# Kernel tuning notes

Measured on AMD Instinct MI355X. Metric: run time of the kernel, lower is better.

Reference implementation:

```python
import jax, jax.numpy as jnp
import numpy as np

DEPTH = 4
DIM = 1024
HEADS = 16
DIM_HEAD = 64
BLOCK = 128
FF_HID = 2730  # int(1024 * 4.0 * 2 / 3)
EPS = 1.1920929e-07  # torch float32 finfo eps (nn.RMSNorm default)
SCALE = DIM_HEAD ** -0.5


def rmsnorm(x, w):
    return x * jax.lax.rsqrt(jnp.mean(x * x, axis=-1, keepdims=True) + EPS) * w


def rope(x):
    # interleaved rotary embedding (rotary-embedding-torch convention)
    n, d = x.shape[-2], x.shape[-1]
    freqs = 1.0 / (10000.0 ** (jnp.arange(0, d, 2, dtype=jnp.float32) / d))  # [d/2]
    ang = jnp.arange(n, dtype=jnp.float32)[:, None] * freqs                  # [n, d/2]
    cos = jnp.repeat(jnp.cos(ang), 2, axis=-1)  # [n, d], interleaved
    sin = jnp.repeat(jnp.sin(ang), 2, axis=-1)
    xp = x.reshape(x.shape[:-1] + (d // 2, 2))
    xr = jnp.stack((-xp[..., 1], xp[..., 0]), axis=-1).reshape(x.shape)
    return x * cos + xr * sin


def setup_inputs() -> dict:
    key = jax.random.key(0)
    ks = jax.random.split(key, 8)
    g = lambda k, shape: jax.random.normal(k, shape, jnp.float32) * 0.02
    return dict(
        tokens=jax.random.normal(ks[0], (1, 2048, DIM), jnp.float32),
        attn_norm_w=jnp.ones((DEPTH, DIM), jnp.float32),
        w_qkv=g(ks[1], (DEPTH, DIM, 3 * HEADS * DIM_HEAD)),
        w_attn_out=g(ks[2], (DEPTH, HEADS * DIM_HEAD, DIM)),
        w_mix=g(ks[3], (DEPTH, DIM, HEADS)),
        b_mix=jnp.zeros((DEPTH, HEADS), jnp.float32),
        ff_norm_w=jnp.ones((DEPTH, DIM), jnp.float32),
        w_ff_in=g(ks[4], (DEPTH, DIM, 2 * FF_HID)),
        b_ff_in=jnp.zeros((DEPTH, 2 * FF_HID), jnp.float32),
        w_ff_out=g(ks[5], (DEPTH, FF_HID, DIM)),
        b_ff_out=jnp.zeros((DEPTH, DIM), jnp.float32),
        final_norm_w=jnp.ones((DIM,), jnp.float32),
    )


def reference(tokens, attn_norm_w, w_qkv, w_attn_out, w_mix, b_mix,
              ff_norm_w, w_ff_in, b_ff_in, w_ff_out, b_ff_out, final_norm_w):
    b, n, _ = tokens.shape
    qi = jnp.arange(n) // BLOCK
    mask = qi[:, None] >= qi[None, :]  # block-causal [n, n]
    neg = -jnp.finfo(jnp.float32).max

    def split_heads(t):
        return t.reshape(b, n, HEADS, DIM_HEAD).transpose(0, 2, 1, 3)  # b h n d

    x = tokens
    first_v = None
    for i in range(DEPTH):
        # --- block-causal attention ---
        h = rmsnorm(x, attn_norm_w[i])
        q, k, v = jnp.split(h @ w_qkv[i], 3, axis=-1)
        q, k, v = split_heads(q), split_heads(k), split_heads(v)
        orig_v = v
        q, k = rope(q), rope(k)
        if first_v is not None:
            mix = jax.nn.sigmoid(h @ w_mix[i] + b_mix[i])      # b n h
            mix = mix.transpose(0, 2, 1)[..., None]            # b h n 1
            v = v + mix * (first_v - v)                        # lerp
        sim = jnp.einsum('bhid,bhjd->bhij', q * SCALE, k)
        sim = jnp.where(mask, sim, neg)
        attn = jax.nn.softmax(sim, axis=-1)
        o = jnp.einsum('bhij,bhjd->bhid', attn, v)
        o = o.transpose(0, 2, 1, 3).reshape(b, n, HEADS * DIM_HEAD)
        x = x + o @ w_attn_out[i]
        if first_v is None:
            first_v = orig_v
        # --- SwiGLU feedforward ---
        hf = rmsnorm(x, ff_norm_w[i])
        a, g_ = jnp.split(hf @ w_ff_in[i] + b_ff_in[i], 2, axis=-1)
        x = x + (a * jax.nn.gelu(g_, approximate=False)) @ w_ff_out[i] + b_ff_out[i]

    return rmsnorm(x, final_norm_w)
```

## Files before the change

kernel.cpp:

```cpp
#include <hip/hip_runtime.h>
#include <hip/hip_bf16.h>

#define DIM   1024
#define NTOK  2048
#define HEADS 16
#define FFH   2730
#define FF2   5460
#define FFHP  2752
#define FFNP  2816
#define DEPTH 4
#define EPS_RMS 1.1920929e-07f
#define QK_SCALE 0.125f

typedef __attribute__((ext_vector_type(8))) short bf16x8;
typedef __attribute__((ext_vector_type(4))) float f32x4;

__device__ __forceinline__ unsigned short f2bf(float x) {
    unsigned u = __float_as_uint(x);
    u += 0x7fffu + ((u >> 16) & 1);
    return (unsigned short)(u >> 16);
}
__device__ __forceinline__ float bf2f(unsigned short u) {
    return __uint_as_float((unsigned)u << 16);
}
__device__ __forceinline__ unsigned pk2(float a, float b) {
    unsigned ua = __float_as_uint(a); ua += 0x7fffu + ((ua >> 16) & 1);
    unsigned ub = __float_as_uint(b); ub += 0x7fffu + ((ub >> 16) & 1);
    return (ua >> 16) | (ub & 0xffff0000u);
}
__device__ __forceinline__ void gll16(const void* g, void* l) {
    __builtin_amdgcn_global_load_lds(
        (const __attribute__((address_space(1))) void*)g,
        (__attribute__((address_space(3))) void*)l, 16, 0, 0);
}

__global__ void rmsnorm_k(const float* __restrict__ in, const float* __restrict__ w,
                          unsigned short* __restrict__ outbf) {
    int row = blockIdx.x;
    int tid = threadIdx.x;
    const float4* in4 = (const float4*)(in + (size_t)row * DIM);
    float4 v = in4[tid];
    float ss = v.x * v.x + v.y * v.y + v.z * v.z + v.w * v.w;
    #pragma unroll
    for (int off = 32; off > 0; off >>= 1) ss += __shfl_down(ss, off);
    __shared__ float lds[4];
    __shared__ float stot;
    int wid = tid >> 6, lane = tid & 63;
    if (lane == 0) lds[wid] = ss;
    __syncthreads();
    if (tid == 0) stot = lds[0] + lds[1] + lds[2] + lds[3];
    __syncthreads();
    float inv = 1.0f / sqrtf(stot * (1.0f / DIM) + EPS_RMS);
    const float4* w4 = (const float4*)w;
    float4 wv = w4[tid];
    float4 o;
    o.x = v.x * inv * wv.x; o.y = v.y * inv * wv.y;
    o.z = v.z * inv * wv.z; o.w = v.w * inv * wv.w;
    unsigned long long p = (unsigned long long)pk2(o.x, o.y)
                         | ((unsigned long long)pk2(o.z, o.w) << 32);
    ((unsigned long long*)(outbf + (size_t)row * DIM))[tid] = p;
}

template<int S, int DOMIX>
__global__ void rmsnorm_red_k(const float* __restrict__ X,
                              const unsigned short* __restrict__ P,
                              const float* __restrict__ bias, const float* __restrict__ w,
                              float* __restrict__ Xout, float* __restrict__ Hf,
                              unsigned short* __restrict__ Hbf,
                              const float* __restrict__ wm, const float* __restrict__ bm,
                              float* __restrict__ mix) {
    int row = blockIdx.x;
    int tid = threadIdx.x;
    float4 x = ((const float4*)(X + (size_t)row * DIM))[tid];
    #pragma unroll
    for (int s = 0; s < S; s++) {
        ushort4 p = ((const ushort4*)(P + (size_t)s * NTOK * DIM + (size_t)row * DIM))[tid];
        x.x += bf2f(p.x); x.y += bf2f(p.y); x.z += bf2f(p.z); x.w += bf2f(p.w);
    }
    if (bias) {
        float4 b = ((const float4*)bias)[tid];
        x.x += b.x; x.y += b.y; x.z += b.z; x.w += b.w;
    }
    float ss = x.x * x.x + x.y * x.y + x.z * x.z + x.w * x.w;
    #pragma unroll
    for (int off = 32; off > 0; off >>= 1) ss += __shfl_down(ss, off);
    __shared__ float lds[4];
    __shared__ float stot;
    int wid = tid >> 6, lane = tid & 63;
    if (lane == 0) lds[wid] = ss;
    __syncthreads();
    if (tid == 0) stot = lds[0] + lds[1] + lds[2] + lds[3];
    __syncthreads();
    float inv = 1.0f / sqrtf(stot * (1.0f / DIM) + EPS_RMS);
    if (Xout) ((float4*)(Xout + (size_t)row * DIM))[tid] = x;
    float4 wv = ((const float4*)w)[tid];
    float4 o;
    o.x = x.x * inv * wv.x; o.y = x.y * inv * wv.y;
    o.z = x.z * inv * wv.z; o.w = x.w * inv * wv.w;
    if (Hf) ((float4*)(Hf + (size_t)row * DIM))[tid] = o;
    if (Hbf) {
        unsigned long long p = (unsigned long long)pk2(o.x, o.y)
                             | ((unsigned long long)pk2(o.z, o.w) << 32);
        ((unsigned long long*)(Hbf + (size_t)row * DIM))[tid] = p;
    }
    if (DOMIX) {
        __shared__ float olds[1024];
        __shared__ float red[256];
        ((float4*)olds)[tid] = o;
        __syncthreads();
        int hh = tid & 15, kl = tid >> 4;
        float pm = 0.f;
        #pragma unroll
        for (int j = 0; j < 64; j++) {
            int k = kl + 16 * j;
            pm += olds[k] * wm[k * 16 + hh];
        }
        red[tid] = pm;
        __syncthreads();
        if (tid < 16) {
            float s = 0.f;
            #pragma unroll
            for (int k2 = 0; k2 < 16; k2++) s += red[k2 * 16 + tid];
            s += bm[tid];
            mix[row * HEADS + tid] = 1.0f / (1.0f + expf(-s));
        }
    }
}

__global__ __launch_bounds__(256) void wconv_k(
        const float* __restrict__ W0, short* __restrict__ out0,
        int Ksrc, int Nsrc, int colOfs, int rowStride, int Kp, int Np,
        size_t wStride, size_t oStride) {
    const float* W = W0 + (size_t)blockIdx.z * wStride;
    short* out = out0 + (size_t)blockIdx.z * oStride;
    __shared__ float tile[64][65];
    int k0 = blockIdx.y * 64, n0 = blockIdx.x * 64;
    int tid = threadIdx.x;
    int c = tid & 63;
    #pragma unroll
    for (int kk4 = 0; kk4 < 16; kk4++) {
        int kk = kk4 * 4 + (tid >> 6);
        int gk = k0 + kk, gn = n0 + c;
        float v = 0.f;
        if (gk < Ksrc && gn < Nsrc) v = W[(size_t)gk * rowStride + colOfs + gn];
        tile[kk][c] = v;
    }
    __syncthreads();
    #pragma unroll
    for (int it = 0; it < 4; it++) {
        int flat = tid + 256 * it;
        int nn = flat >> 4, kg = (flat & 15) * 4;
        int gn = n0 + nn, gk = k0 + kg;
        if (gn < Np && gk < Kp) {
            short4 s;
            s.x = (short)f2bf(tile[kg + 0][nn]);
            s.y = (short)f2bf(tile[kg + 1][nn]);
            s.z = (short)f2bf(tile[kg + 2][nn]);
            s.w = (short)f2bf(tile[kg + 3][nn]);
            *(short4*)(out + (size_t)gn * Kp + gk) = s;
        }
    }
}

template<int SPLITK, int OUT16>
__global__ __launch_bounds__(256, 2) void gemm_splitk_k(
        const short* __restrict__ A, const short* __restrict__ Bt,
        void* __restrict__ Cpart, int N, int Kp) {
    __shared__ __align__(16) short As[128 * 64];
    __shared__ __align__(16) short Bs[128 * 64];
    int tid = threadIdx.x;
    int wv = tid >> 6, ln = tid & 63, g = ln >> 4, t = ln & 15;
    int wr = wv >> 1, wc = wv & 1;
    int rowBase = blockIdx.y * 128, colBase = blockIdx.x * 128;
    f32x4 acc[4][4] = {};
    int KT = Kp >> 6;
    int kt0 = (KT * blockIdx.z) / SPLITK, kt1 = (KT * (blockIdx.z + 1)) / SPLITK;
    for (int kt = kt0; kt < kt1; kt++) {
        int k0 = kt * 64;
        #pragma unroll
        for (int i = 0; i < 4; i++) {
            int idx = tid + 256 * i;
            int r = idx >> 3, c8 = idx & 7;
            int cs = (c8 ^ (r & 7)) * 8;
            gll16(A + (size_t)(rowBase + r) * Kp + k0 + cs, (char*)As + idx * 16);
            gll16(Bt + (size_t)(colBase + r) * Kp + k0 + cs, (char*)Bs + idx * 16);
        }
        __syncthreads();
        #pragma unroll
        for (int ks = 0; ks < 2; ks++) {
            bf16x8 af[4], bf[4];
            #pragma unroll
            for (int mi = 0; mi < 4; mi++) {
                int row = wr * 64 + mi * 16 + t;
                int kb = (ks * 64 + g * 16) ^ ((row & 7) << 4);
                af[mi] = *(const bf16x8*)((const char*)As + row * 128 + kb);
            }
            #pragma unroll
            for (int ni = 0; ni < 4; ni++) {
                int row = wc * 64 + ni * 16 + t;
                int kb = (ks * 64 + g * 16) ^ ((row & 7) << 4);
                bf[ni] = *(const bf16x8*)((const char*)Bs + row * 128 + kb);
            }
            #pragma unroll
            for (int mi = 0; mi < 4; mi++)
                #pragma unroll
                for (int ni = 0; ni < 4; ni++)
                    acc[mi][ni] = __builtin_amdgcn_mfma_f32_16x16x32_bf16(
                        af[mi], bf[ni], acc[mi][ni], 0, 0, 0);
        }
        __syncthreads();
    }
    #pragma unroll
    for (int mi = 0; mi < 4; mi++)
        #pragma unroll
        for (int ni = 0; ni < 4; ni++) {
            int col = colBase + wc * 64 + ni * 16 + t;
            #pragma unroll
            for (int r = 0; r < 4; r++) {
                int row = rowBase + wr * 64 + mi * 16 + g * 4 + r;
                if (OUT16) {
                    unsigned short* Cz = (unsigned short*)Cpart
                                       + (size_t)blockIdx.z * NTOK * N;
                    Cz[(size_t)row * N + col] = f2bf(acc[mi][ni][r]);
                } else {
                    float* Cz = (float*)Cpart + (size_t)blockIdx.z * NTOK * N;
                    Cz[(size_t)row * N + col] = acc[mi][ni][r];
                }
            }
        }
}

__global__ __launch_bounds__(256, 2) void gemm_swiglu_k(
        const short* __restrict__ A, const short* __restrict__ Ba,
        const short* __restrict__ Bg, const float* __restrict__ biasIn,
        unsigned short* __restrict__ actbf) {
    __shared__ __align__(16) short As[128 * 64];
    __shared__ __align__(16) short B1[128 * 64];
    __shared__ __align__(16) short B2[128 * 64];
    int tid = threadIdx.x;
    int wv = tid >> 6, ln = tid & 63, g = ln >> 4, t = ln & 15;
    int wr = wv >> 1, wc = wv & 1;
    int rowBase = blockIdx.y * 128, colBase = blockIdx.x * 128;
    f32x4 acca[4][4] = {};
    f32x4 accg[4][4] = {};
    for (int kt = 0; kt < 16; kt++) {
        int k0 = kt * 64;
        #pragma unroll
        for (int i = 0; i < 4; i++) {
            int idx = tid + 256 * i;
            int r = idx >> 3, c8 = idx & 7;
            int cs = (c8 ^ (r & 7)) * 8;
            gll16(A + (size_t)(rowBase + r) * 1024 + k0 + cs, (char*)As + idx * 16);
            gll16(Ba + (size_t)(colBase + r) * 1024 + k0 + cs, (char*)B1 + idx * 16);
            gll16(Bg + (size_t)(colBase + r) * 1024 + k0 + cs, (char*)B2 + idx * 16);
        }
        __syncthreads();
        #pragma unroll
        for (int ks = 0; ks < 2; ks++) {
            bf16x8 af[4], b1f[4], b2f[4];
            #pragma unroll
            for (int mi = 0; mi < 4; mi++) {
                int row = wr * 64 + mi * 16 + t;
                int kb = (ks * 64 + g * 16) ^ ((row & 7) << 4);
                af[mi] = *(const bf16x8*)((const char*)As + row * 128 + kb);
            }
            #pragma unroll
            for (int ni = 0; ni < 4; ni++) {
                int row = wc * 64 + ni * 16 + t;
                int kb = (ks * 64 + g * 16) ^ ((row & 7) << 4);
                b1f[ni] = *(const bf16x8*)((const char*)B1 + row * 128 + kb);
                b2f[ni] = *(const bf16x8*)((const char*)B2 + row * 128 + kb);
            }
            #pragma unroll
            for (int mi = 0; mi < 4; mi++)
                #pragma unroll
                for (int ni = 0; ni < 4; ni++) {
                    acca[mi][ni] = __builtin_amdgcn_mfma_f32_16x16x32_bf16(
                        af[mi], b1f[ni], acca[mi][ni], 0, 0, 0);
                    accg[mi][ni] = __builtin_amdgcn_mfma_f32_16x16x32_bf16(
                        af[mi], b2f[ni], accg[mi][ni], 0, 0, 0);
                }
        }
        __syncthreads();
    }
    const float rs2 = 0.70710678118654752f;
    #pragma unroll
    for (int mi = 0; mi < 4; mi++)
        #pragma unroll
        for (int ni = 0; ni < 4; ni++) {
            int col = colBase + wc * 64 + ni * 16 + t;
            if (col < FFHP) {
                float ba = (col < FFH) ? biasIn[col] : 0.f;
                float bg = (col < FFH) ? biasIn[FFH + col] : 0.f;
                #pragma unroll
                for (int r = 0; r < 4; r++) {
                    int row = rowBase + wr * 64 + mi * 16 + g * 4 + r;
                    unsigned short outv = 0;
                    if (col < FFH) {
                        float a_ = acca[mi][ni][r] + ba;
                        float g_ = accg[mi][ni][r] + bg;
                        float gel = 0.5f * g_ * (1.0f + erff(g_ * rs2));
                        outv = f2bf(a_ * gel);
                    }
                    actbf[(size_t)row * FFHP + col] = outv;
                }
            }
        }
}

__global__ void rope_lerp_k(const float* __restrict__ qkv,
                            unsigned short* __restrict__ qbf,
                            unsigned short* __restrict__ kbf) {
    int row = blockIdx.x;
    int tid = threadIdx.x;
    const float* qr = qkv + (size_t)row * 3072;
    #pragma unroll
    for (int it = 0; it < 2; it++) {
        int p = tid + 256 * it;
        int hh = p >> 5, pr = p & 31;
        float freq = expf(-(float)pr * (1.0f / 32.0f) * 9.2103403719762f);
        float ang = (float)row * freq;
        float s, c;
        sincosf(ang, &s, &c);
        int base = hh * 64 + pr * 2;
        float q0 = qr[base], q1 = qr[base + 1];
        float qa = q0 * c - q1 * s, qb = q1 * c + q0 * s;
        *(unsigned*)(qbf + (size_t)row * DIM + base) = pk2(qa * QK_SCALE, qb * QK_SCALE);
        float k0 = qr[1024 + base], k1 = qr[1024 + base + 1];
        *(unsigned*)(kbf + (size_t)row * DIM + base) = pk2(k0 * c - k1 * s, k1 * c + k0 * s);
    }
}

__global__ __launch_bounds__(256) void vtrans_k(
        const float* __restrict__ qkv, float* __restrict__ fv,
        const float* __restrict__ mix, unsigned short* __restrict__ vtg, int layer) {
    __shared__ __align__(16) short T[64 * 64];
    int h = blockIdx.x, n0 = blockIdx.y * 64;
    int tid = threadIdx.x;
    #pragma unroll
    for (int it = 0; it < 2; it++) {
        int flat = tid + 256 * it;
        int n = flat >> 3, d0 = (flat & 7) * 8;
        int row = n0 + n;
        const float* src = qkv + (size_t)row * 3072 + 2048 + h * 64 + d0;
        float4 u0 = *(const float4*)src;
        float4 u1 = *(const float4*)(src + 4);
        float vals[8] = {u0.x, u0.y, u0.z, u0.w, u1.x, u1.y, u1.z, u1.w};
        float* fvp = fv + (size_t)row * DIM + h * 64 + d0;
        if (layer == 0) {
            *(float4*)fvp = u0;
            *(float4*)(fvp + 4) = u1;
        } else {
            float m = mix[row * HEADS + h];
            float4 f0 = *(const float4*)fvp;
            float4 f1 = *(const float4*)(fvp + 4);
            float fvv[8] = {f0.x, f0.y, f0.z, f0.w, f1.x, f1.y, f1.z, f1.w};
            #pragma unroll
            for (int e = 0; e < 8; e++) vals[e] += m * (fvv[e] - vals[e]);
        }
        #pragma unroll
        for (int e = 0; e < 8; e++) {
            int d = d0 + e;
            *(short*)((char*)T + d * 128 + ((2 * n) ^ ((d & 7) << 4))) = (short)f2bf(vals[e]);
        }
    }
    __syncthreads();
    #pragma unroll
    for (int it = 0; it < 2; it++) {
        int flat = tid + 256 * it;
        int d = flat >> 3, nn0 = (flat & 7) * 8;
        uint4 v = *(const uint4*)((const char*)T + d * 128 + ((2 * nn0) ^ ((d & 7) << 4)));
        *(uint4*)(vtg + (size_t)(h * 64 + d) * NTOK + n0 + nn0) = v;
    }
}

__global__ __launch_bounds__(256, 2) void attn_mfma_k(
        const unsigned short* __restrict__ Qbf, const unsigned short* __restrict__ Kbf,
        const unsigned short* __restrict__ Vtg, unsigned short* __restrict__ obf) {
    const int h = blockIdx.x;
    const int j = 31 - (int)blockIdx.y;
    const int tid = threadIdx.x;
    const int wv = tid >> 6, ln = tid & 63, g = ln >> 4, t = ln & 15;
    __shared__ __align__(16) short KsB[2][64 * 64];
    __shared__ __align__(16) short VtB[2][64 * 64];
    __shared__ __align__(16) short Plds[4 * 16 * 64];
    char* pw = (char*)(Plds + wv * 1024);

    const int sr = ln >> 3;
    const int scol = (ln & 7) ^ sr;
    const int sbyte0 = (wv * 16 + sr) * 128 + (ln & 7) * 16;
    const int sbyte1 = sbyte0 + 8 * 128;
    const unsigned short* kgl0 = Kbf + (size_t)(wv * 16 + sr) * DIM + h * 64 + scol * 8;
    const unsigned short* kgl1 = kgl0 + 8 * DIM;
    const unsigned short* vgl0 = Vtg + (size_t)(h * 64 + wv * 16 + sr) * NTOK + scol * 8;
    const unsigned short* vgl1 = vgl0 + 8 * NTOK;

    const int nch = ((j >> 1) + 1) * 2;
    const int qbase = j * 64;
    const unsigned short* qrow = Qbf + (size_t)(qbase + wv * 16 + t) * DIM + h * 64;
    bf16x8 qf0 = *(const bf16x8*)(qrow + 8 * g);
    bf16x8 qf1 = *(const bf16x8*)(qrow + 32 + 8 * g);
    f32x4 acc_o[4] = {};
    float mrun = -3.0e38f, lrun = 0.f;
    uint4 rk0 = *(const uint4*)kgl0;
    uint4 rk1 = *(const uint4*)kgl1;
    uint4 rv0 = *(const uint4*)vgl0;
    uint4 rv1 = *(const uint4*)vgl1;
    for (int kc = 0; kc < nch; kc++) {
        const int cur = kc & 1;
        *(uint4*)((char*)KsB[cur] + sbyte0) = rk0;
        *(uint4*)((char*)KsB[cur] + sbyte1) = rk1;
        *(uint4*)((char*)VtB[cur] + sbyte0) = rv0;
        *(uint4*)((char*)VtB[cur] + sbyte1) = rv1;
        if (kc + 1 < nch) {
            rk0 = *(const uint4*)(kgl0 + (size_t)(kc + 1) * 64 * DIM);
            rk1 = *(const uint4*)(kgl1 + (size_t)(kc + 1) * 64 * DIM);
            rv0 = *(const uint4*)(vgl0 + (kc + 1) * 64);
            rv1 = *(const uint4*)(vgl1 + (kc + 1) * 64);
        }
        __syncthreads();
        const char* Kc = (const char*)KsB[cur];
        const char* Vc = (const char*)VtB[cur];
        f32x4 accs[4] = {};
        #pragma unroll
        for (int kf = 0; kf < 4; kf++) {
            int row = kf * 16 + t;
            int kb0 = (g * 16) ^ ((row & 7) << 4);
            int kb1 = (64 + g * 16) ^ ((row & 7) << 4);
            bf16x8 k0 = *(const bf16x8*)(Kc + row * 128 + kb0);
            bf16x8 k1 = *(const bf16x8*)(Kc + row * 128 + kb1);
            accs[kf] = __builtin_amdgcn_mfma_f32_16x16x32_bf16(k0, qf0, accs[kf], 0, 0, 0);
            accs[kf] = __builtin_amdgcn_mfma_f32_16x16x32_bf16(k1, qf1, accs[kf], 0, 0, 0);
        }
        float pm = -3.0e38f;
        #pragma unroll
        for (int kf = 0; kf < 4; kf++)
            #pragma unroll
            for (int r = 0; r < 4; r++) pm = fmaxf(pm, accs[kf][r]);
        pm = fmaxf(pm, __shfl_xor(pm, 16));
        pm = fmaxf(pm, __shfl_xor(pm, 32));
        float mnew = fmaxf(mrun, pm);
        float corr = __expf(mrun - mnew);
        mrun = mnew;
        float psum = 0.f;
        #pragma unroll
        for (int kf = 0; kf < 4; kf++)
            #pragma unroll
            for (int r = 0; r < 4; r++) {
                float pv = __expf(accs[kf][r] - mnew);
                accs[kf][r] = pv;
                psum += pv;
            }
        psum += __shfl_xor(psum, 16);
        psum += __shfl_xor(psum, 32);
        lrun = lrun * corr + psum;
        #pragma unroll
        for (int kf = 0; kf < 4; kf++)
            #pragma unroll
            for (int rp = 0; rp < 4; rp += 2) {
                unsigned pv = pk2(accs[kf][rp], accs[kf][rp + 1]);
                int boff = (t * 128 + (16 * kf + 4 * g + rp) * 2) ^ ((t & 7) << 4);
                *(unsigned*)(pw + boff) = pv;
            }
        float cr[4];
        #pragma unroll
        for (int r = 0; r < 4; r++) cr[r] = __shfl(corr, g * 4 + r);
        #pragma unroll
        for (int ni = 0; ni < 4; ni++)
            #pragma unroll
            for (int r = 0; r < 4; r++) acc_o[ni][r] *= cr[r];
        #pragma unroll
        for (int ks = 0; ks < 2; ks++) {
            bf16x8 pa = *(const bf16x8*)(pw + ((t * 128 + 64 * ks + 16 * g) ^ ((t & 7) << 4)));
            #pragma unroll
            for (int ni = 0; ni < 4; ni++) {
                int row = ni * 16 + t;
                int vb = (64 * ks + 16 * g) ^ ((row & 7) << 4);
                bf16x8 vbf = *(const bf16x8*)(Vc + row * 128 + vb);
                acc_o[ni] = __builtin_amdgcn_mfma_f32_16x16x32_bf16(pa, vbf, acc_o[ni], 0, 0, 0);
            }
        }
    }
    float inv = 1.0f / lrun;
    float ir[4];
    #pragma unroll
    for (int r = 0; r < 4; r++) ir[r] = __shfl(inv, g * 4 + r);
    #pragma unroll
    for (int ni = 0; ni < 4; ni++)
        #pragma unroll
        for (int r = 0; r < 4; r++) {
            int row = qbase + wv * 16 + g * 4 + r;
            int col = h * 64 + ni * 16 + t;
            obf[(size_t)row * DIM + col] = f2bf(acc_o[ni][r] * ir[r]);
        }
}

extern "C" void kernel_launch(void* const* d_in, const int* in_sizes, int n_in,
                              void* d_out, int out_size, void* d_ws, size_t ws_size,
                              hipStream_t stream) {
    const float* tokens       = (const float*)d_in[0];
    const float* attn_norm_w  = (const float*)d_in[1];
    const float* w_qkv        = (const float*)d_in[2];
    const float* w_attn_out   = (const float*)d_in[3];
    const float* w_mix        = (const float*)d_in[4];
    const float* b_mix        = (const float*)d_in[5];
    const float* ff_norm_w    = (const float*)d_in[6];
    const float* b_ff_in      = (const float*)d_in[8];
    const float* w_ff_in      = (const float*)d_in[7];
    const float* w_ff_out     = (const float*)d_in[9];
    const float* b_ff_out     = (const float*)d_in[10];
    const float* final_norm_w = (const float*)d_in[11];

    char* p = (char*)d_ws;
    auto alloc = [&](size_t bytes) {
        char* r = p;
        p += (bytes + 255) & ~(size_t)255;
        return r;
    };
    short* wq_t  = (short*)alloc(4ull * 3072 * 1024 * 2);
    short* wo_t  = (short*)alloc(4ull * 1024 * 1024 * 2);
    short* wfa_t = (short*)alloc(4ull * FFNP * 1024 * 2);
    short* wfg_t = (short*)alloc(4ull * FFNP * 1024 * 2);
    short* wfo_t = (short*)alloc(4ull * 1024 * FFHP * 2);
    float* PART  = (float*)alloc((size_t)NTOK * 3072 * 4);
    float* X     = (float*)alloc((size_t)NTOK * DIM * 4);
    float* FV    = (float*)alloc((size_t)NTOK * DIM * 4);
    float* MIX   = (float*)alloc((size_t)NTOK * HEADS * 4);
    short* Hbf   = (short*)alloc((size_t)NTOK * DIM * 2);
    short* Obf   = (short*)alloc((size_t)NTOK * DIM * 2);
    short* ACTbf = (short*)alloc((size_t)NTOK * FFHP * 2);
    unsigned short* Qbf = (unsigned short*)alloc((size_t)NTOK * DIM * 2);
    unsigned short* Kbf = (unsigned short*)alloc((size_t)NTOK * DIM * 2);
    unsigned short* Vtg = (unsigned short*)alloc((size_t)HEADS * 64 * NTOK * 2);
    float* QKVf = PART;
    unsigned short* PARTb = (unsigned short*)PART;

    wconv_k<<<dim3(48, 16, 4), 256, 0, stream>>>(
        w_qkv, wq_t, 1024, 3072, 0, 3072, 1024, 3072,
        (size_t)1024 * 3072, (size_t)3072 * 1024);
    wconv_k<<<dim3(16, 16, 4), 256, 0, stream>>>(
        w_attn_out, wo_t, 1024, 1024, 0, 1024, 1024, 1024,
        (size_t)1024 * 1024, (size_t)1024 * 1024);
    wconv_k<<<dim3(44, 16, 4), 256, 0, stream>>>(
        w_ff_in, wfa_t, 1024, FFH, 0, FF2, 1024, FFNP,
        (size_t)1024 * FF2, (size_t)FFNP * 1024);
    wconv_k<<<dim3(44, 16, 4), 256, 0, stream>>>(
        w_ff_in, wfg_t, 1024, FFH, FFH, FF2, 1024, FFNP,
        (size_t)1024 * FF2, (size_t)FFNP * 1024);
    wconv_k<<<dim3(16, 43, 4), 256, 0, stream>>>(
        w_ff_out, wfo_t, FFH, 1024, 0, 1024, FFHP, 1024,
        (size_t)FFH * 1024, (size_t)1024 * FFHP);

    hipMemcpyAsync(X, tokens, (size_t)NTOK * DIM * sizeof(float),
                   hipMemcpyDeviceToDevice, stream);
    rmsnorm_k<<<NTOK, 256, 0, stream>>>(X, attn_norm_w, (unsigned short*)Hbf);

    for (int i = 0; i < DEPTH; i++) {
        gemm_splitk_k<1, 0><<<dim3(24, 16, 1), 256, 0, stream>>>(
            Hbf, wq_t + (size_t)i * 3072 * 1024, QKVf, 3072, 1024);
        rope_lerp_k<<<NTOK, 256, 0, stream>>>(QKVf, Qbf, Kbf);
        vtrans_k<<<dim3(16, 32), 256, 0, stream>>>(QKVf, FV, MIX, Vtg, i);
        attn_mfma_k<<<dim3(16, 32), 256, 0, stream>>>(Qbf, Kbf, Vtg,
                                                      (unsigned short*)Obf);
        gemm_splitk_k<4, 1><<<dim3(8, 16, 4), 256, 0, stream>>>(
            Obf, wo_t + (size_t)i * 1024 * 1024, PARTb, 1024, 1024);
        rmsnorm_red_k<4, 0><<<NTOK, 256, 0, stream>>>(
            X, PARTb, nullptr, ff_norm_w + (size_t)i * DIM, X, nullptr,
            (unsigned short*)Hbf, nullptr, nullptr, nullptr);
        gemm_swiglu_k<<<dim3(22, 16), 256, 0, stream>>>(
            Hbf, wfa_t + (size_t)i * FFNP * 1024, wfg_t + (size_t)i * FFNP * 1024,
            b_ff_in + (size_t)i * FF2, (unsigned short*)ACTbf);
        gemm_splitk_k<4, 1><<<dim3(8, 16, 4), 256, 0, stream>>>(
            ACTbf, wfo_t + (size_t)i * 1024 * FFHP, PARTb, 1024, FFHP);
        if (i < DEPTH - 1) {
            rmsnorm_red_k<4, 1><<<NTOK, 256, 0, stream>>>(
                X, PARTb, b_ff_out + (size_t)i * DIM, attn_norm_w + (size_t)(i + 1) * DIM,
                X, nullptr, (unsigned short*)Hbf,
                w_mix + (size_t)(i + 1) * DIM * HEADS, b_mix + (size_t)(i + 1) * HEADS,
                MIX);
        } else {
            rmsnorm_red_k<4, 0><<<NTOK, 256, 0, stream>>>(
                X, PARTb, b_ff_out + (size_t)i * DIM, final_norm_w,
                nullptr, (float*)d_out, nullptr, nullptr, nullptr, nullptr);
        }
    }
}
```

Baseline: 757.0 us.

## Split-K QKV GEMM into bf16 partials, narrow SwiGLU tiles, raise occupancy

The QKV projection now runs as a 2-way split-K GEMM that writes bf16 partials. rope_lerp_k and vtrans_k sum the two partials on load, where before they read a single fp32 output. The SwiGLU GEMM tile is narrowed from 128 to 64 columns, so the grid grows from 22 to 43 column blocks and each block needs fewer registers and less LDS, and both GEMM kernels ask for 4 blocks per CU instead of 2. The aim is to fill more CUs and keep more waves resident on these small-grid GEMMs, at the cost of rounding the QKV result to bf16 before RoPE and of more A-tile reloads in SwiGLU.

After: 716.0 us. -5.4%, faster.

```diff
diff --git a/kernel.cpp b/kernel.cpp
--- a/kernel.cpp
+++ b/kernel.cpp
@@ -27,6 +27,12 @@
     unsigned ua = __float_as_uint(a); ua += 0x7fffu + ((ua >> 16) & 1);
     unsigned ub = __float_as_uint(b); ub += 0x7fffu + ((ub >> 16) & 1);
     return (ua >> 16) | (ub & 0xffff0000u);
+}
+__device__ __forceinline__ void unpk8(uint4 u, float* v) {
+    v[0] = bf2f((unsigned short)u.x); v[1] = bf2f((unsigned short)(u.x >> 16));
+    v[2] = bf2f((unsigned short)u.y); v[3] = bf2f((unsigned short)(u.y >> 16));
+    v[4] = bf2f((unsigned short)u.z); v[5] = bf2f((unsigned short)(u.z >> 16));
+    v[6] = bf2f((unsigned short)u.w); v[7] = bf2f((unsigned short)(u.w >> 16));
 }
 __device__ __forceinline__ void gll16(const void* g, void* l) {
     __builtin_amdgcn_global_load_lds(
@@ -163,7 +169,7 @@
 }
 
 template<int SPLITK, int OUT16>
-__global__ __launch_bounds__(256, 2) void gemm_splitk_k(
+__global__ __launch_bounds__(256, 4) void gemm_splitk_k(
         const short* __restrict__ A, const short* __restrict__ Bt,
         void* __restrict__ Cpart, int N, int Kp) {
     __shared__ __align__(16) short As[128 * 64];
@@ -230,19 +236,19 @@
         }
 }
 
-__global__ __launch_bounds__(256, 2) void gemm_swiglu_k(
+__global__ __launch_bounds__(256, 4) void gemm_swiglu_k(
         const short* __restrict__ A, const short* __restrict__ Ba,
         const short* __restrict__ Bg, const float* __restrict__ biasIn,
         unsigned short* __restrict__ actbf) {
     __shared__ __align__(16) short As[128 * 64];
-    __shared__ __align__(16) short B1[128 * 64];
-    __shared__ __align__(16) short B2[128 * 64];
+    __shared__ __align__(16) short B1[64 * 64];
+    __shared__ __align__(16) short B2[64 * 64];
     int tid = threadIdx.x;
     int wv = tid >> 6, ln = tid & 63, g = ln >> 4, t = ln & 15;
     int wr = wv >> 1, wc = wv & 1;
-    int rowBase = blockIdx.y * 128, colBase = blockIdx.x * 128;
-    f32x4 acca[4][4] = {};
-    f32x4 accg[4][4] = {};
+    int rowBase = blockIdx.y * 128, colBase = blockIdx.x * 64;
+    f32x4 acca[4][2] = {};
+    f32x4 accg[4][2] = {};
     for (int kt = 0; kt < 16; kt++) {
         int k0 = kt * 64;
         #pragma unroll
@@ -251,13 +257,19 @@
             int r = idx >> 3, c8 = idx & 7;
             int cs = (c8 ^ (r & 7)) * 8;
             gll16(A + (size_t)(rowBase + r) * 1024 + k0 + cs, (char*)As + idx * 16);
+        }
+        #pragma unroll
+        for (int i = 0; i < 2; i++) {
+            int idx = tid + 256 * i;
+            int r = idx >> 3, c8 = idx & 7;
+            int cs = (c8 ^ (r & 7)) * 8;
             gll16(Ba + (size_t)(colBase + r) * 1024 + k0 + cs, (char*)B1 + idx * 16);
             gll16(Bg + (size_t)(colBase + r) * 1024 + k0 + cs, (char*)B2 + idx * 16);
         }
         __syncthreads();
         #pragma unroll
         for (int ks = 0; ks < 2; ks++) {
-            bf16x8 af[4], b1f[4], b2f[4];
+            bf16x8 af[4], b1f[2], b2f[2];
             #pragma unroll
             for (int mi = 0; mi < 4; mi++) {
                 int row = wr * 64 + mi * 16 + t;
@@ -265,8 +277,8 @@
                 af[mi] = *(const bf16x8*)((const char*)As + row * 128 + kb);
             }
             #pragma unroll
-            for (int ni = 0; ni < 4; ni++) {
-                int row = wc * 64 + ni * 16 + t;
+            for (int ni = 0; ni < 2; ni++) {
+                int row = wc * 32 + ni * 16 + t;
                 int kb = (ks * 64 + g * 16) ^ ((row & 7) << 4);
                 b1f[ni] = *(const bf16x8*)((const char*)B1 + row * 128 + kb);
                 b2f[ni] = *(const bf16x8*)((const char*)B2 + row * 128 + kb);
@@ -274,7 +286,7 @@
             #pragma unroll
             for (int mi = 0; mi < 4; mi++)
                 #pragma unroll
-                for (int ni = 0; ni < 4; ni++) {
+                for (int ni = 0; ni < 2; ni++) {
                     acca[mi][ni] = __builtin_amdgcn_mfma_f32_16x16x32_bf16(
                         af[mi], b1f[ni], acca[mi][ni], 0, 0, 0);
                     accg[mi][ni] = __builtin_amdgcn_mfma_f32_16x16x32_bf16(
@@ -287,33 +299,32 @@
     #pragma unroll
     for (int mi = 0; mi < 4; mi++)
         #pragma unroll
-        for (int ni = 0; ni < 4; ni++) {
-            int col = colBase + wc * 64 + ni * 16 + t;
-            if (col < FFHP) {
-                float ba = (col < FFH) ? biasIn[col] : 0.f;
-                float bg = (col < FFH) ? biasIn[FFH + col] : 0.f;
-                #pragma unroll
-                for (int r = 0; r < 4; r++) {
-                    int row = rowBase + wr * 64 + mi * 16 + g * 4 + r;
-                    unsigned short outv = 0;
-                    if (col < FFH) {
-                        float a_ = acca[mi][ni][r] + ba;
-                        float g_ = accg[mi][ni][r] + bg;
-                        float gel = 0.5f * g_ * (1.0f + erff(g_ * rs2));
-                        outv = f2bf(a_ * gel);
-                    }
-                    actbf[(size_t)row * FFHP + col] = outv;
+        for (int ni = 0; ni < 2; ni++) {
+            int col = colBase + wc * 32 + ni * 16 + t;
+            float ba = (col < FFH) ? biasIn[col] : 0.f;
+            float bg = (col < FFH) ? biasIn[FFH + col] : 0.f;
+            #pragma unroll
+            for (int r = 0; r < 4; r++) {
+                int row = rowBase + wr * 64 + mi * 16 + g * 4 + r;
+                unsigned short outv = 0;
+                if (col < FFH) {
+                    float a_ = acca[mi][ni][r] + ba;
+                    float g_ = accg[mi][ni][r] + bg;
+                    float gel = 0.5f * g_ * (1.0f + erff(g_ * rs2));
+                    outv = f2bf(a_ * gel);
                 }
-            }
-        }
-}
-
-__global__ void rope_lerp_k(const float* __restrict__ qkv,
+                actbf[(size_t)row * FFHP + col] = outv;
+            }
+        }
+}
+
+__global__ void rope_lerp_k(const unsigned short* __restrict__ P,
                             unsigned short* __restrict__ qbf,
                             unsigned short* __restrict__ kbf) {
     int row = blockIdx.x;
     int tid = threadIdx.x;
-    const float* qr = qkv + (size_t)row * 3072;
+    const unsigned short* s0 = P + (size_t)row * 3072;
+    const unsigned short* s1 = s0 + (size_t)NTOK * 3072;
     #pragma unroll
     for (int it = 0; it < 2; it++) {
         int p = tid + 256 * it;
@@ -323,16 +334,22 @@
         float s, c;
         sincosf(ang, &s, &c);
         int base = hh * 64 + pr * 2;
-        float q0 = qr[base], q1 = qr[base + 1];
+        unsigned a0 = *(const unsigned*)(s0 + base);
+        unsigned a1 = *(const unsigned*)(s1 + base);
+        float q0 = bf2f((unsigned short)a0) + bf2f((unsigned short)a1);
+        float q1 = bf2f((unsigned short)(a0 >> 16)) + bf2f((unsigned short)(a1 >> 16));
         float qa = q0 * c - q1 * s, qb = q1 * c + q0 * s;
         *(unsigned*)(qbf + (size_t)row * DIM + base) = pk2(qa * QK_SCALE, qb * QK_SCALE);
-        float k0 = qr[1024 + base], k1 = qr[1024 + base + 1];
+        unsigned b0 = *(const unsigned*)(s0 + 1024 + base);
+        unsigned b1 = *(const unsigned*)(s1 + 1024 + base);
+        float k0 = bf2f((unsigned short)b0) + bf2f((unsigned short)b1);
+        float k1 = bf2f((unsigned short)(b0 >> 16)) + bf2f((unsigned short)(b1 >> 16));
         *(unsigned*)(kbf + (size_t)row * DIM + base) = pk2(k0 * c - k1 * s, k1 * c + k0 * s);
     }
 }
 
 __global__ __launch_bounds__(256) void vtrans_k(
-        const float* __restrict__ qkv, float* __restrict__ fv,
+        const unsigned short* __restrict__ P, float* __restrict__ fv,
         const float* __restrict__ mix, unsigned short* __restrict__ vtg, int layer) {
     __shared__ __align__(16) short T[64 * 64];
     int h = blockIdx.x, n0 = blockIdx.y * 64;
@@ -342,14 +359,17 @@
         int flat = tid + 256 * it;
         int n = flat >> 3, d0 = (flat & 7) * 8;
         int row = n0 + n;
-        const float* src = qkv + (size_t)row * 3072 + 2048 + h * 64 + d0;
-        float4 u0 = *(const float4*)src;
-        float4 u1 = *(const float4*)(src + 4);
-        float vals[8] = {u0.x, u0.y, u0.z, u0.w, u1.x, u1.y, u1.z, u1.w};
+        const unsigned short* s0 = P + (size_t)row * 3072 + 2048 + h * 64 + d0;
+        const unsigned short* s1 = s0 + (size_t)NTOK * 3072;
+        float a[8], b[8], vals[8];
+        unpk8(*(const uint4*)s0, a);
+        unpk8(*(const uint4*)s1, b);
+        #pragma unroll
+        for (int e = 0; e < 8; e++) vals[e] = a[e] + b[e];
         float* fvp = fv + (size_t)row * DIM + h * 64 + d0;
         if (layer == 0) {
-            *(float4*)fvp = u0;
-            *(float4*)(fvp + 4) = u1;
+            *(float4*)fvp = make_float4(vals[0], vals[1], vals[2], vals[3]);
+            *(float4*)(fvp + 4) = make_float4(vals[4], vals[5], vals[6], vals[7]);
         } else {
             float m = mix[row * HEADS + h];
             float4 f0 = *(const float4*)fvp;
@@ -505,8 +525,8 @@
     const float* w_mix        = (const float*)d_in[4];
     const float* b_mix        = (const float*)d_in[5];
     const float* ff_norm_w    = (const float*)d_in[6];
+    const float* w_ff_in      = (const float*)d_in[7];
     const float* b_ff_in      = (const float*)d_in[8];
-    const float* w_ff_in      = (const float*)d_in[7];
     const float* w_ff_out     = (const float*)d_in[9];
     const float* b_ff_out     = (const float*)d_in[10];
     const float* final_norm_w = (const float*)d_in[11];
@@ -532,7 +552,7 @@
     unsigned short* Qbf = (unsigned short*)alloc((size_t)NTOK * DIM * 2);
     unsigned short* Kbf = (unsigned short*)alloc((size_t)NTOK * DIM * 2);
     unsigned short* Vtg = (unsigned short*)alloc((size_t)HEADS * 64 * NTOK * 2);
-    float* QKVf = PART;
+    unsigned short* PARTq = (unsigned short*)PART;
     unsigned short* PARTb = (unsigned short*)PART;
 
     wconv_k<<<dim3(48, 16, 4), 256, 0, stream>>>(
@@ -556,10 +576,10 @@
     rmsnorm_k<<<NTOK, 256, 0, stream>>>(X, attn_norm_w, (unsigned short*)Hbf);
 
     for (int i = 0; i < DEPTH; i++) {
-        gemm_splitk_k<1, 0><<<dim3(24, 16, 1), 256, 0, stream>>>(
-            Hbf, wq_t + (size_t)i * 3072 * 1024, QKVf, 3072, 1024);
-        rope_lerp_k<<<NTOK, 256, 0, stream>>>(QKVf, Qbf, Kbf);
-        vtrans_k<<<dim3(16, 32), 256, 0, stream>>>(QKVf, FV, MIX, Vtg, i);
+        gemm_splitk_k<2, 1><<<dim3(24, 16, 2), 256, 0, stream>>>(
+            Hbf, wq_t + (size_t)i * 3072 * 1024, PARTq, 3072, 1024);
+        rope_lerp_k<<<NTOK, 256, 0, stream>>>(PARTq, Qbf, Kbf);
+        vtrans_k<<<dim3(16, 32), 256, 0, stream>>>(PARTq, FV, MIX, Vtg, i);
         attn_mfma_k<<<dim3(16, 32), 256, 0, stream>>>(Qbf, Kbf, Vtg,
                                                       (unsigned short*)Obf);
         gemm_splitk_k<4, 1><<<dim3(8, 16, 4), 256, 0, stream>>>(
@@ -567,7 +587,7 @@
         rmsnorm_red_k<4, 0><<<NTOK, 256, 0, stream>>>(
             X, PARTb, nullptr, ff_norm_w + (size_t)i * DIM, X, nullptr,
             (unsigned short*)Hbf, nullptr, nullptr, nullptr);
-        gemm_swiglu_k<<<dim3(22, 16), 256, 0, stream>>>(
+        gemm_swiglu_k<<<dim3(43, 16), 256, 0, stream>>>(
             Hbf, wfa_t + (size_t)i * FFNP * 1024, wfg_t + (size_t)i * FFNP * 1024,
             b_ff_in + (size_t)i * FF2, (unsigned short*)ACTbf);
         gemm_splitk_k<4, 1><<<dim3(8, 16, 4), 256, 0, stream>>>(
```
